# Performance work log

Measured on AMD Instinct MI355X. Metric: run time of the kernel, lower is better.

The kernel has to match this reference:

```python
import jax, jax.numpy as jnp
import numpy as np

N = 100000      # kg_E, number of entities
D = 256         # rel_dim
E = 1600000     # total COO edges (all batches concatenated)


def setup_inputs() -> dict:
    key = jax.random.key(0)
    ks = jax.random.split(key, 8)
    right_embed = jax.random.normal(ks[0], (N, D), dtype=jnp.float32)
    W1 = jax.random.normal(ks[1], (D, D), dtype=jnp.float32) * 0.02
    Wr = jax.random.normal(ks[2], (D, D), dtype=jnp.float32) * 0.02
    br = jax.random.normal(ks[3], (D,), dtype=jnp.float32) * 0.02
    edge_vals = jax.random.uniform(ks[4], (E,), dtype=jnp.float32)  # 1/(deg+1) weights
    edge_rows = jnp.sort(jax.random.randint(ks[5], (E,), 0, N))
    edge_cols = jax.random.randint(ks[6], (E,), 0, N)
    perm = jax.random.randint(ks[7], (N,), 0, N)  # ent_newid_tensor
    return {"right_embed": right_embed, "W1": W1, "Wr": Wr, "br": br,
            "edge_vals": edge_vals, "edge_rows": edge_rows,
            "edge_cols": edge_cols, "perm": perm}


def reference(right_embed, W1, Wr, br, edge_vals, edge_rows, edge_cols, perm):
    # add_diag_layer: dense transform then normalized-adjacency SpMM + ReLU
    h = right_embed @ W1                                   # [N, D]
    msg = edge_vals[:, None] * h[edge_cols]                # [E, D] gather
    agg = jax.ops.segment_sum(msg, edge_rows, num_segments=N)  # scatter-add
    gcn_e_1 = jax.nn.relu(agg)                             # [N, D]
    # highway gate blend with permuted input embeddings
    left = right_embed[perm]                               # [N, D]
    gate = jax.nn.sigmoid(left @ Wr + br)                  # [N, D]
    return gate * gcn_e_1 + (1.0 - gate) * left
```

## Files before the change

### kernel.cpp

```cpp
#include <hip/hip_runtime.h>
#include <hip/hip_bf16.h>
#include <math.h>

#define D 256

typedef short s16x8 __attribute__((ext_vector_type(8)));
typedef float f32x4 __attribute__((ext_vector_type(4)));

__device__ __forceinline__ unsigned short f2bf(float f) {
    unsigned int u = __builtin_bit_cast(unsigned int, f);
    unsigned int r = (u + 0x7fffu + ((u >> 16) & 1u)) >> 16;
    return (unsigned short)r;
}
__device__ __forceinline__ float bf2f(unsigned short s) {
    unsigned int u = ((unsigned int)s) << 16;
    return __builtin_bit_cast(float, u);
}

__global__ void swizzle_w(const float* __restrict__ W1, const float* __restrict__ Wr,
                          unsigned short* __restrict__ W1sw, unsigned short* __restrict__ Wrsw) {
    int idx = blockIdx.x * blockDim.x + threadIdx.x;
    int m = idx >> 16;
    int t = idx & 65535;
    const float* src = m ? Wr : W1;
    unsigned short* dst = m ? Wrsw : W1sw;
    int j = t & 7, lane = (t >> 3) & 63, nt = (t >> 9) & 15, kt = t >> 13;
    int k = kt * 32 + (lane >> 4) * 8 + j;
    int n = nt * 16 + (lane & 15);
    dst[t] = f2bf(src[k * D + n]);
}

__global__ void build_row_ptr(const int* __restrict__ rows, int* __restrict__ rp, int N, int E) {
    int r = blockIdx.x * blockDim.x + threadIdx.x;
    if (r > N) return;
    int lo = 0, hi = E;
    while (lo < hi) {
        int mid = (lo + hi) >> 1;
        if (rows[mid] < r) lo = mid + 1; else hi = mid;
    }
    rp[r] = lo;
}


__device__ __forceinline__ void stage_a_frag(const float* __restrict__ Xrow, int k0,
                                             unsigned short* __restrict__ lA, int fgi) {
    float4 f0 = *(const float4*)(Xrow + k0);
    float4 f1 = *(const float4*)(Xrow + k0 + 4);
    s16x8 sf;
    sf[0] = (short)f2bf(f0.x); sf[1] = (short)f2bf(f0.y);
    sf[2] = (short)f2bf(f0.z); sf[3] = (short)f2bf(f0.w);
    sf[4] = (short)f2bf(f1.x); sf[5] = (short)f2bf(f1.y);
    sf[6] = (short)f2bf(f1.z); sf[7] = (short)f2bf(f1.w);
    *(s16x8*)(lA + (size_t)fgi * 8) = sf;
}

__global__ __launch_bounds__(512) void gemm1_b(const float* __restrict__ X,
                                               const unsigned short* __restrict__ Wsw,
                                               unsigned short* __restrict__ h,
                                               int N, int numTiles) {
    __shared__ unsigned short lA[2 * 8 * 64 * 8];
    int t = threadIdx.x;
    int lane = t & 63;
    int wave = t >> 6;
    int quad = lane >> 4;

    s16x8 bfr[2][8];
#pragma unroll
    for (int ntl = 0; ntl < 2; ntl++) {
        int nt = wave * 2 + ntl;
#pragma unroll
        for (int kt = 0; kt < 8; kt++)
            bfr[ntl][kt] = *(const s16x8*)(Wsw + ((size_t)((kt * 16 + nt) * 64 + lane)) * 8);
    }

    for (int tile = blockIdx.x; tile < numTiles; tile += gridDim.x) {
#pragma unroll
        for (int q = 0; q < 2; q++) {
            int fgi = q * 512 + t;
            int mt = fgi >> 9, kt = (fgi >> 6) & 7, ll = fgi & 63;
            int rl = ll & 15, qd = ll >> 4;
            int grow = tile * 32 + mt * 16 + rl;
            if (grow >= N) grow = N - 1;
            stage_a_frag(X + (size_t)grow * D, kt * 32 + qd * 8, lA, fgi);
        }
        __syncthreads();

        f32x4 acc[2][2];
#pragma unroll
        for (int mt = 0; mt < 2; mt++)
#pragma unroll
            for (int ntl = 0; ntl < 2; ntl++) acc[mt][ntl] = (f32x4){0.f, 0.f, 0.f, 0.f};

#pragma unroll
        for (int mt = 0; mt < 2; mt++)
#pragma unroll
            for (int kt = 0; kt < 8; kt++) {
                s16x8 a = *(const s16x8*)(lA + (size_t)(((mt * 8 + kt) * 64 + lane)) * 8);
                acc[mt][0] = __builtin_amdgcn_mfma_f32_16x16x32_bf16(a, bfr[0][kt], acc[mt][0], 0, 0, 0);
                acc[mt][1] = __builtin_amdgcn_mfma_f32_16x16x32_bf16(a, bfr[1][kt], acc[mt][1], 0, 0, 0);
            }

#pragma unroll
        for (int mt = 0; mt < 2; mt++)
#pragma unroll
            for (int ntl = 0; ntl < 2; ntl++) {
                int col = (wave * 2 + ntl) * 16 + (lane & 15);
#pragma unroll
                for (int r = 0; r < 4; r++) {
                    int grow = tile * 32 + mt * 16 + quad * 4 + r;
                    if (grow < N) h[(size_t)grow * D + col] = f2bf(acc[mt][ntl][r]);
                }
            }
        __syncthreads();
    }
}

__global__ __launch_bounds__(512) void gemm2_b(const float* __restrict__ X,
                                               const int* __restrict__ perm,
                                               const unsigned short* __restrict__ Wsw,
                                               const float* __restrict__ br,
                                               const unsigned short* __restrict__ agg,
                                               float* __restrict__ out,
                                               int N, int numTiles) {
    __shared__ unsigned short lA[2 * 8 * 64 * 8];
    int t = threadIdx.x;
    int lane = t & 63;
    int wave = t >> 6;
    int quad = lane >> 4;

    s16x8 bfr[2][8];
#pragma unroll
    for (int ntl = 0; ntl < 2; ntl++) {
        int nt = wave * 2 + ntl;
#pragma unroll
        for (int kt = 0; kt < 8; kt++)
            bfr[ntl][kt] = *(const s16x8*)(Wsw + ((size_t)((kt * 16 + nt) * 64 + lane)) * 8);
    }

    for (int tile = blockIdx.x; tile < numTiles; tile += gridDim.x) {
#pragma unroll
        for (int q = 0; q < 2; q++) {
            int fgi = q * 512 + t;
            int mt = fgi >> 9, kt = (fgi >> 6) & 7, ll = fgi & 63;
            int rl = ll & 15, qd = ll >> 4;
            int grow = tile * 32 + mt * 16 + rl;
            if (grow >= N) grow = N - 1;
            int pr = perm[grow];
            stage_a_frag(X + (size_t)pr * D, kt * 32 + qd * 8, lA, fgi);
        }
        __syncthreads();

        f32x4 acc[2][2];
#pragma unroll
        for (int mt = 0; mt < 2; mt++)
#pragma unroll
            for (int ntl = 0; ntl < 2; ntl++) acc[mt][ntl] = (f32x4){0.f, 0.f, 0.f, 0.f};

#pragma unroll
        for (int mt = 0; mt < 2; mt++)
#pragma unroll
            for (int kt = 0; kt < 8; kt++) {
                s16x8 a = *(const s16x8*)(lA + (size_t)(((mt * 8 + kt) * 64 + lane)) * 8);
                acc[mt][0] = __builtin_amdgcn_mfma_f32_16x16x32_bf16(a, bfr[0][kt], acc[mt][0], 0, 0, 0);
                acc[mt][1] = __builtin_amdgcn_mfma_f32_16x16x32_bf16(a, bfr[1][kt], acc[mt][1], 0, 0, 0);
            }

#pragma unroll
        for (int mt = 0; mt < 2; mt++) {
#pragma unroll
            for (int ntl = 0; ntl < 2; ntl++) {
                int col = (wave * 2 + ntl) * 16 + (lane & 15);
                float b = br[col];
                int kt2 = col >> 5, qd2 = (col >> 3) & 3, j2 = col & 7;
#pragma unroll
                for (int r = 0; r < 4; r++) {
                    int rt = mt * 16 + quad * 4 + r;
                    int grow = tile * 32 + rt;
                    if (grow < N) {
                        float pre = acc[mt][ntl][r] + b;
                        float gate = 1.f / (1.f + __expf(-pre));
                        float gcn = bf2f(agg[(size_t)grow * D + col]);
                        float left = bf2f(lA[(size_t)(((mt * 8 + kt2) * 64 + qd2 * 16 + (rt & 15))) * 8 + j2]);
                        out[(size_t)grow * D + col] = gate * gcn + (1.f - gate) * left;
                    }
                }
            }
        }
        __syncthreads();
    }
}

__device__ __forceinline__ void acc4(float4& a, uint2 u, float v) {
    float x0 = __builtin_bit_cast(float, u.x << 16);
    float x1 = __builtin_bit_cast(float, u.x & 0xffff0000u);
    float x2 = __builtin_bit_cast(float, u.y << 16);
    float x3 = __builtin_bit_cast(float, u.y & 0xffff0000u);
    a.x += v * x0; a.y += v * x1; a.z += v * x2; a.w += v * x3;
}

__global__ __launch_bounds__(256) void scatter2(const uint2* __restrict__ hp,
                                                const int* __restrict__ rp,
                                                const int* __restrict__ cols,
                                                const float* __restrict__ vals,
                                                uint2* __restrict__ aggp,
                                                int N, int E) {
    int lane = threadIdx.x & 63;
    int wave = threadIdx.x >> 6;
    int row = blockIdx.x * 4 + wave;
    if (row >= N) return;
    int start = rp[row], end = rp[row + 1];

    float4 a = {0.f, 0.f, 0.f, 0.f};
    for (int base = start; base < end; base += 64) {
        int ii = base + lane;
        int iic = ii < E ? ii : E - 1;
        int cl = cols[iic];
        int vbits = __builtin_bit_cast(int, vals[iic]);
        int n = end - base; if (n > 64) n = 64;
        int i = 0;
        for (; i + 8 <= n; i += 8) {
            uint2 u[8]; float vv[8];
#pragma unroll
            for (int k = 0; k < 8; k++) {
                int c = __builtin_amdgcn_readlane(cl, i + k);
                vv[k] = __builtin_bit_cast(float, __builtin_amdgcn_readlane(vbits, i + k));
                u[k] = hp[(size_t)c * 64 + lane];
            }
#pragma unroll
            for (int k = 0; k < 8; k++) acc4(a, u[k], vv[k]);
        }
        for (; i < n; i++) {
            int c = __builtin_amdgcn_readlane(cl, i);
            float v = __builtin_bit_cast(float, __builtin_amdgcn_readlane(vbits, i));
            uint2 u = hp[(size_t)c * 64 + lane];
            acc4(a, u, v);
        }
    }
    a.x = fmaxf(a.x, 0.f); a.y = fmaxf(a.y, 0.f);
    a.z = fmaxf(a.z, 0.f); a.w = fmaxf(a.w, 0.f);
    uint2 o;
    o.x = (unsigned int)f2bf(a.x) | ((unsigned int)f2bf(a.y) << 16);
    o.y = (unsigned int)f2bf(a.z) | ((unsigned int)f2bf(a.w) << 16);
    aggp[(size_t)row * 64 + lane] = o;
}

extern "C" void kernel_launch(void* const* d_in, const int* in_sizes, int n_in,
                              void* d_out, int out_size, void* d_ws, size_t ws_size,
                              hipStream_t stream) {
    const float* right = (const float*)d_in[0];
    const float* W1    = (const float*)d_in[1];
    const float* Wr    = (const float*)d_in[2];
    const float* br    = (const float*)d_in[3];
    const float* evals = (const float*)d_in[4];
    const int*   erows = (const int*)d_in[5];
    const int*   ecols = (const int*)d_in[6];
    const int*   perm  = (const int*)d_in[7];
    int N = in_sizes[7];
    int E = in_sizes[4];
    float* out = (float*)d_out;

    char* ws = (char*)d_ws;
    unsigned short* W1sw = (unsigned short*)ws;
    unsigned short* Wrsw = W1sw + D * D;
    int* rp = (int*)(ws + (size_t)2 * D * D * 2);
    size_t off = (size_t)2 * D * D * 2 + 4 * (size_t)(N + 1);
    off = (off + 255) & ~(size_t)255;
    unsigned short* h = (unsigned short*)(ws + off);
    unsigned short* agg = h + (size_t)N * D;

    int numTiles = (N + 31) / 32;

    swizzle_w<<<512, 256, 0, stream>>>(W1, Wr, W1sw, Wrsw);
    build_row_ptr<<<(N + 256) / 256, 256, 0, stream>>>(erows, rp, N, E);
    gemm1_b<<<numTiles, 512, 0, stream>>>(right, W1sw, h, N, numTiles);
    scatter2<<<(N + 3) / 4, 256, 0, stream>>>((const uint2*)h, rp, ecols, evals,
                                              (uint2*)agg, N, E);
    gemm2_b<<<numTiles, 512, 0, stream>>>(right, perm, Wrsw, br, agg, out, N, numTiles);
}
```

Before: 417.1 us.

## Store h and agg in column-group-major layout and scatter per column group

The intermediate h and agg buffers change from row-major to 16 column groups of 16 bf16 values each, stored group-major. The SpMM kernel is split so each block handles one column group, with eight edges per wave processed in parallel and combined by a shuffle reduction. Block IDs are interleaved so groups map to different XCDs, keeping each group's 3.2 MB slice of h in L2. Each gather now moves 32 bytes per edge instead of 512, at the cost of reading the edge arrays 16 times and extra shuffle work. The GEMM grids are also capped at 768 persistent blocks.

Result: slower. 633.5 us (+51.9%).

```diff
diff --git a/kernel.cpp b/kernel.cpp
--- a/kernel.cpp
+++ b/kernel.cpp
@@ -104,11 +104,13 @@
         for (int mt = 0; mt < 2; mt++)
 #pragma unroll
             for (int ntl = 0; ntl < 2; ntl++) {
-                int col = (wave * 2 + ntl) * 16 + (lane & 15);
+                int g = wave * 2 + ntl;
+                int c = lane & 15;
 #pragma unroll
                 for (int r = 0; r < 4; r++) {
                     int grow = tile * 32 + mt * 16 + quad * 4 + r;
-                    if (grow < N) h[(size_t)grow * D + col] = f2bf(acc[mt][ntl][r]);
+                    if (grow < N)
+                        h[(size_t)g * N * 16 + (size_t)grow * 16 + c] = f2bf(acc[mt][ntl][r]);
                 }
             }
         __syncthreads();
@@ -169,7 +171,9 @@
         for (int mt = 0; mt < 2; mt++) {
 #pragma unroll
             for (int ntl = 0; ntl < 2; ntl++) {
-                int col = (wave * 2 + ntl) * 16 + (lane & 15);
+                int g = wave * 2 + ntl;
+                int cc = lane & 15;
+                int col = g * 16 + cc;
                 float b = br[col];
                 int kt2 = col >> 5, qd2 = (col >> 3) & 3, j2 = col & 7;
 #pragma unroll
@@ -179,7 +183,7 @@
                     if (grow < N) {
                         float pre = acc[mt][ntl][r] + b;
                         float gate = 1.f / (1.f + __expf(-pre));
-                        float gcn = bf2f(agg[(size_t)grow * D + col]);
+                        float gcn = bf2f(agg[(size_t)g * N * 16 + (size_t)grow * 16 + cc]);
                         float left = bf2f(lA[(size_t)(((mt * 8 + kt2) * 64 + qd2 * 16 + (rt & 15))) * 8 + j2]);
                         out[(size_t)grow * D + col] = gate * gcn + (1.f - gate) * left;
                     }
@@ -190,58 +194,55 @@
     }
 }
 
-__device__ __forceinline__ void acc4(float4& a, uint2 u, float v) {
-    float x0 = __builtin_bit_cast(float, u.x << 16);
-    float x1 = __builtin_bit_cast(float, u.x & 0xffff0000u);
-    float x2 = __builtin_bit_cast(float, u.y << 16);
-    float x3 = __builtin_bit_cast(float, u.y & 0xffff0000u);
-    a.x += v * x0; a.y += v * x1; a.z += v * x2; a.w += v * x3;
-}
-
-__global__ __launch_bounds__(256) void scatter2(const uint2* __restrict__ hp,
+__global__ __launch_bounds__(256) void scatter3(const unsigned int* __restrict__ hg,
                                                 const int* __restrict__ rp,
                                                 const int* __restrict__ cols,
                                                 const float* __restrict__ vals,
-                                                uint2* __restrict__ aggp,
-                                                int N, int E) {
+                                                unsigned int* __restrict__ aggg,
+                                                int N, int E, int BPG) {
+    int bid = blockIdx.x;
+    int x = bid & 7;
+    int j = bid >> 3;
+    int hi = (j >= BPG) ? 1 : 0;
+    int g = 2 * x + hi;
+    int bg = j - hi * BPG;
+    int wave = threadIdx.x >> 6;
     int lane = threadIdx.x & 63;
-    int wave = threadIdx.x >> 6;
-    int row = blockIdx.x * 4 + wave;
-    if (row >= N) return;
-    int start = rp[row], end = rp[row + 1];
-
-    float4 a = {0.f, 0.f, 0.f, 0.f};
-    for (int base = start; base < end; base += 64) {
-        int ii = base + lane;
-        int iic = ii < E ? ii : E - 1;
-        int cl = cols[iic];
-        int vbits = __builtin_bit_cast(int, vals[iic]);
-        int n = end - base; if (n > 64) n = 64;
-        int i = 0;
-        for (; i + 8 <= n; i += 8) {
-            uint2 u[8]; float vv[8];
-#pragma unroll
-            for (int k = 0; k < 8; k++) {
-                int c = __builtin_amdgcn_readlane(cl, i + k);
-                vv[k] = __builtin_bit_cast(float, __builtin_amdgcn_readlane(vbits, i + k));
-                u[k] = hp[(size_t)c * 64 + lane];
-            }
-#pragma unroll
-            for (int k = 0; k < 8; k++) acc4(a, u[k], vv[k]);
-        }
-        for (; i < n; i++) {
-            int c = __builtin_amdgcn_readlane(cl, i);
-            float v = __builtin_bit_cast(float, __builtin_amdgcn_readlane(vbits, i));
-            uint2 u = hp[(size_t)c * 64 + lane];
-            acc4(a, u, v);
-        }
-    }
-    a.x = fmaxf(a.x, 0.f); a.y = fmaxf(a.y, 0.f);
-    a.z = fmaxf(a.z, 0.f); a.w = fmaxf(a.w, 0.f);
-    uint2 o;
-    o.x = (unsigned int)f2bf(a.x) | ((unsigned int)f2bf(a.y) << 16);
-    o.y = (unsigned int)f2bf(a.z) | ((unsigned int)f2bf(a.w) << 16);
-    aggp[(size_t)row * 64 + lane] = o;
+    int s = lane >> 3;
+    int ci = lane & 7;
+    const unsigned int* hbase = hg + (size_t)g * N * 8;
+    unsigned int* abase = aggg + (size_t)g * N * 8;
+    int stride = BPG * 4;
+    for (int row = bg * 4 + wave; row < N; row += stride) {
+        int start = rp[row], end = rp[row + 1];
+        float a0 = 0.f, a1 = 0.f;
+        for (int base = start; base < end; base += 64) {
+            int ii = base + lane;
+            int iic = ii < E ? ii : E - 1;
+            int cl = cols[iic];
+            int vb = __builtin_bit_cast(int, vals[iic]);
+            int n = end - base; if (n > 64) n = 64;
+            for (int i = 0; i < n; i += 8) {
+                int idx = (i + s) << 2;
+                int c = __builtin_amdgcn_ds_bpermute(idx, cl);
+                int vvb = __builtin_amdgcn_ds_bpermute(idx, vb);
+                float v = (i + s) < n ? __builtin_bit_cast(float, vvb) : 0.f;
+                unsigned int u = hbase[(size_t)c * 8 + ci];
+                float x0 = __builtin_bit_cast(float, u << 16);
+                float x1 = __builtin_bit_cast(float, u & 0xffff0000u);
+                a0 += v * x0;
+                a1 += v * x1;
+            }
+        }
+        a0 += __shfl_xor(a0, 8, 64);  a1 += __shfl_xor(a1, 8, 64);
+        a0 += __shfl_xor(a0, 16, 64); a1 += __shfl_xor(a1, 16, 64);
+        a0 += __shfl_xor(a0, 32, 64); a1 += __shfl_xor(a1, 32, 64);
+        if (s == 0) {
+            a0 = fmaxf(a0, 0.f); a1 = fmaxf(a1, 0.f);
+            unsigned int o = (unsigned int)f2bf(a0) | ((unsigned int)f2bf(a1) << 16);
+            abase[(size_t)row * 8 + ci] = o;
+        }
+    }
 }
 
 extern "C" void kernel_launch(void* const* d_in, const int* in_sizes, int n_in,
@@ -269,11 +270,13 @@
     unsigned short* agg = h + (size_t)N * D;
 
     int numTiles = (N + 31) / 32;
+    int gemmGrid = numTiles < 768 ? numTiles : 768;
+    int BPG = 1024;
 
     swizzle_w<<<512, 256, 0, stream>>>(W1, Wr, W1sw, Wrsw);
     build_row_ptr<<<(N + 256) / 256, 256, 0, stream>>>(erows, rp, N, E);
-    gemm1_b<<<numTiles, 512, 0, stream>>>(right, W1sw, h, N, numTiles);
-    scatter2<<<(N + 3) / 4, 256, 0, stream>>>((const uint2*)h, rp, ecols, evals,
-                                              (uint2*)agg, N, E);
-    gemm2_b<<<numTiles, 512, 0, stream>>>(right, perm, Wrsw, br, agg, out, N, numTiles);
-}
+    gemm1_b<<<gemmGrid, 512, 0, stream>>>(right, W1sw, h, N, numTiles);
+    scatter3<<<16 * BPG, 256, 0, stream>>>((const unsigned int*)h, rp, ecols, evals,
+                                           (unsigned int*)agg, N, E, BPG);
+    gemm2_b<<<gemmGrid, 512, 0, stream>>>(right, perm, Wrsw, br, agg, out, N, numTiles);
+}
```

## Pre-pack bf16 A tiles and double-buffer them into LDS with async loads

Applied to the files above, without the earlier changes.

Adds a pack_x kernel that converts the fp32 input rows (gathered through perm for the gate GEMM) into bf16 MFMA-fragment-ordered tiles in workspace. Both GEMMs become persistent kernels with a grid capped at 512 that stream these packed tiles into double-buffered LDS using global_load_lds, so the next tile's load overlaps the current tile's MFMAs. The goal is to hide load latency and drop per-tile conversion and perm indexing from the GEMM loops. In exchange it adds two extra kernels and an extra write and read of a bf16 copy of the input, with workspace buffers aliased to hold it.

New measurement: 413.9 us. No clear change (-0.8%).

```diff
diff --git a/kernel.cpp b/kernel.cpp
--- a/kernel.cpp
+++ b/kernel.cpp
@@ -15,6 +15,12 @@
 __device__ __forceinline__ float bf2f(unsigned short s) {
     unsigned int u = ((unsigned int)s) << 16;
     return __builtin_bit_cast(float, u);
+}
+
+__device__ __forceinline__ void gl_lds16(const unsigned short* g, unsigned short* l) {
+    __builtin_amdgcn_global_load_lds(
+        (const __attribute__((address_space(1))) unsigned int*)g,
+        (__attribute__((address_space(3))) unsigned int*)l, 16, 0, 0);
 }
 
 __global__ void swizzle_w(const float* __restrict__ W1, const float* __restrict__ Wr,
@@ -41,9 +47,8 @@
     rp[r] = lo;
 }
 
-
 __device__ __forceinline__ void stage_a_frag(const float* __restrict__ Xrow, int k0,
-                                             unsigned short* __restrict__ lA, int fgi) {
+                                             unsigned short* __restrict__ dst, int fgi) {
     float4 f0 = *(const float4*)(Xrow + k0);
     float4 f1 = *(const float4*)(Xrow + k0 + 4);
     s16x8 sf;
@@ -51,18 +56,35 @@
     sf[2] = (short)f2bf(f0.z); sf[3] = (short)f2bf(f0.w);
     sf[4] = (short)f2bf(f1.x); sf[5] = (short)f2bf(f1.y);
     sf[6] = (short)f2bf(f1.z); sf[7] = (short)f2bf(f1.w);
-    *(s16x8*)(lA + (size_t)fgi * 8) = sf;
-}
-
-__global__ __launch_bounds__(512) void gemm1_b(const float* __restrict__ X,
+    *(s16x8*)(dst + (size_t)fgi * 8) = sf;
+}
+
+__global__ __launch_bounds__(256) void pack_x(const float* __restrict__ X,
+                                              const int* __restrict__ perm,
+                                              unsigned short* __restrict__ Xp,
+                                              int N, int numTiles) {
+    int idx = blockIdx.x * 256 + threadIdx.x;
+    int total = numTiles << 10;
+    if (idx >= total) return;
+    int fgi = idx & 1023, tile = idx >> 10;
+    int mt = fgi >> 9, kt = (fgi >> 6) & 7, ll = fgi & 63;
+    int rl = ll & 15, qd = ll >> 4;
+    int grow = tile * 32 + mt * 16 + rl;
+    if (grow >= N) grow = N - 1;
+    int row = perm ? perm[grow] : grow;
+    stage_a_frag(X + (size_t)row * D, kt * 32 + qd * 8, Xp, idx);
+}
+
+__global__ __launch_bounds__(512) void gemm1_p(const unsigned short* __restrict__ Xp,
                                                const unsigned short* __restrict__ Wsw,
                                                unsigned short* __restrict__ h,
                                                int N, int numTiles) {
-    __shared__ unsigned short lA[2 * 8 * 64 * 8];
+    __shared__ __attribute__((aligned(16))) unsigned short lA[2][8192];
     int t = threadIdx.x;
     int lane = t & 63;
     int wave = t >> 6;
     int quad = lane >> 4;
+    if ((int)blockIdx.x >= numTiles) return;
 
     s16x8 bfr[2][8];
 #pragma unroll
@@ -73,17 +95,26 @@
             bfr[ntl][kt] = *(const s16x8*)(Wsw + ((size_t)((kt * 16 + nt) * 64 + lane)) * 8);
     }
 
-    for (int tile = blockIdx.x; tile < numTiles; tile += gridDim.x) {
-#pragma unroll
-        for (int q = 0; q < 2; q++) {
-            int fgi = q * 512 + t;
-            int mt = fgi >> 9, kt = (fgi >> 6) & 7, ll = fgi & 63;
-            int rl = ll & 15, qd = ll >> 4;
-            int grow = tile * 32 + mt * 16 + rl;
-            if (grow >= N) grow = N - 1;
-            stage_a_frag(X + (size_t)grow * D, kt * 32 + qd * 8, lA, fgi);
-        }
-        __syncthreads();
+    int stride = gridDim.x;
+    int ti = blockIdx.x;
+    {
+        const unsigned short* src = Xp + (size_t)ti * 8192;
+        gl_lds16(src + wave * 512 + lane * 8, &lA[0][wave * 512]);
+        gl_lds16(src + (wave + 8) * 512 + lane * 8, &lA[0][(wave + 8) * 512]);
+    }
+    int cur = 0;
+    for (; ti < numTiles; ti += stride) {
+        int nxt = ti + stride;
+        if (nxt < numTiles) {
+            const unsigned short* src = Xp + (size_t)nxt * 8192;
+            gl_lds16(src + wave * 512 + lane * 8, &lA[cur ^ 1][wave * 512]);
+            gl_lds16(src + (wave + 8) * 512 + lane * 8, &lA[cur ^ 1][(wave + 8) * 512]);
+            asm volatile("s_waitcnt vmcnt(2)" ::: "memory");
+        } else {
+            asm volatile("s_waitcnt vmcnt(0)" ::: "memory");
+        }
+        __builtin_amdgcn_s_barrier();
+        __builtin_amdgcn_sched_barrier(0);
 
         f32x4 acc[2][2];
 #pragma unroll
@@ -95,7 +126,7 @@
         for (int mt = 0; mt < 2; mt++)
 #pragma unroll
             for (int kt = 0; kt < 8; kt++) {
-                s16x8 a = *(const s16x8*)(lA + (size_t)(((mt * 8 + kt) * 64 + lane)) * 8);
+                s16x8 a = *(const s16x8*)(&lA[cur][(size_t)(((mt * 8 + kt) * 64 + lane)) * 8]);
                 acc[mt][0] = __builtin_amdgcn_mfma_f32_16x16x32_bf16(a, bfr[0][kt], acc[mt][0], 0, 0, 0);
                 acc[mt][1] = __builtin_amdgcn_mfma_f32_16x16x32_bf16(a, bfr[1][kt], acc[mt][1], 0, 0, 0);
             }
@@ -107,26 +138,27 @@
                 int col = (wave * 2 + ntl) * 16 + (lane & 15);
 #pragma unroll
                 for (int r = 0; r < 4; r++) {
-                    int grow = tile * 32 + mt * 16 + quad * 4 + r;
+                    int grow = ti * 32 + mt * 16 + quad * 4 + r;
                     if (grow < N) h[(size_t)grow * D + col] = f2bf(acc[mt][ntl][r]);
                 }
             }
-        __syncthreads();
-    }
-}
-
-__global__ __launch_bounds__(512) void gemm2_b(const float* __restrict__ X,
-                                               const int* __restrict__ perm,
+        __builtin_amdgcn_s_barrier();
+        cur ^= 1;
+    }
+}
+
+__global__ __launch_bounds__(512) void gemm2_p(const unsigned short* __restrict__ Xp,
                                                const unsigned short* __restrict__ Wsw,
                                                const float* __restrict__ br,
                                                const unsigned short* __restrict__ agg,
                                                float* __restrict__ out,
                                                int N, int numTiles) {
-    __shared__ unsigned short lA[2 * 8 * 64 * 8];
+    __shared__ __attribute__((aligned(16))) unsigned short lA[2][8192];
     int t = threadIdx.x;
     int lane = t & 63;
     int wave = t >> 6;
     int quad = lane >> 4;
+    if ((int)blockIdx.x >= numTiles) return;
 
     s16x8 bfr[2][8];
 #pragma unroll
@@ -137,18 +169,26 @@
             bfr[ntl][kt] = *(const s16x8*)(Wsw + ((size_t)((kt * 16 + nt) * 64 + lane)) * 8);
     }
 
-    for (int tile = blockIdx.x; tile < numTiles; tile += gridDim.x) {
-#pragma unroll
-        for (int q = 0; q < 2; q++) {
-            int fgi = q * 512 + t;
-            int mt = fgi >> 9, kt = (fgi >> 6) & 7, ll = fgi & 63;
-            int rl = ll & 15, qd = ll >> 4;
-            int grow = tile * 32 + mt * 16 + rl;
-            if (grow >= N) grow = N - 1;
-            int pr = perm[grow];
-            stage_a_frag(X + (size_t)pr * D, kt * 32 + qd * 8, lA, fgi);
-        }
-        __syncthreads();
+    int stride = gridDim.x;
+    int ti = blockIdx.x;
+    {
+        const unsigned short* src = Xp + (size_t)ti * 8192;
+        gl_lds16(src + wave * 512 + lane * 8, &lA[0][wave * 512]);
+        gl_lds16(src + (wave + 8) * 512 + lane * 8, &lA[0][(wave + 8) * 512]);
+    }
+    int cur = 0;
+    for (; ti < numTiles; ti += stride) {
+        int nxt = ti + stride;
+        if (nxt < numTiles) {
+            const unsigned short* src = Xp + (size_t)nxt * 8192;
+            gl_lds16(src + wave * 512 + lane * 8, &lA[cur ^ 1][wave * 512]);
+            gl_lds16(src + (wave + 8) * 512 + lane * 8, &lA[cur ^ 1][(wave + 8) * 512]);
+            asm volatile("s_waitcnt vmcnt(2)" ::: "memory");
+        } else {
+            asm volatile("s_waitcnt vmcnt(0)" ::: "memory");
+        }
+        __builtin_amdgcn_s_barrier();
+        __builtin_amdgcn_sched_barrier(0);
 
         f32x4 acc[2][2];
 #pragma unroll
@@ -160,7 +200,7 @@
         for (int mt = 0; mt < 2; mt++)
 #pragma unroll
             for (int kt = 0; kt < 8; kt++) {
-                s16x8 a = *(const s16x8*)(lA + (size_t)(((mt * 8 + kt) * 64 + lane)) * 8);
+                s16x8 a = *(const s16x8*)(&lA[cur][(size_t)(((mt * 8 + kt) * 64 + lane)) * 8]);
                 acc[mt][0] = __builtin_amdgcn_mfma_f32_16x16x32_bf16(a, bfr[0][kt], acc[mt][0], 0, 0, 0);
                 acc[mt][1] = __builtin_amdgcn_mfma_f32_16x16x32_bf16(a, bfr[1][kt], acc[mt][1], 0, 0, 0);
             }
@@ -175,18 +215,19 @@
 #pragma unroll
                 for (int r = 0; r < 4; r++) {
                     int rt = mt * 16 + quad * 4 + r;
-                    int grow = tile * 32 + rt;
+                    int grow = ti * 32 + rt;
                     if (grow < N) {
                         float pre = acc[mt][ntl][r] + b;
                         float gate = 1.f / (1.f + __expf(-pre));
                         float gcn = bf2f(agg[(size_t)grow * D + col]);
-                        float left = bf2f(lA[(size_t)(((mt * 8 + kt2) * 64 + qd2 * 16 + (rt & 15))) * 8 + j2]);
+                        float left = bf2f(lA[cur][(size_t)(((mt * 8 + kt2) * 64 + qd2 * 16 + (rt & 15))) * 8 + j2]);
                         out[(size_t)grow * D + col] = gate * gcn + (1.f - gate) * left;
                     }
                 }
             }
         }
-        __syncthreads();
+        __builtin_amdgcn_s_barrier();
+        cur ^= 1;
     }
 }
 
@@ -259,6 +300,9 @@
     int E = in_sizes[4];
     float* out = (float*)d_out;
 
+    int numTiles = (N + 31) / 32;
+    size_t tileBytes = (size_t)numTiles * 16384;
+
     char* ws = (char*)d_ws;
     unsigned short* W1sw = (unsigned short*)ws;
     unsigned short* Wrsw = W1sw + D * D;
@@ -266,14 +310,19 @@
     size_t off = (size_t)2 * D * D * 2 + 4 * (size_t)(N + 1);
     off = (off + 255) & ~(size_t)255;
     unsigned short* h = (unsigned short*)(ws + off);
-    unsigned short* agg = h + (size_t)N * D;
-
-    int numTiles = (N + 31) / 32;
+    unsigned short* Xp2 = h;
+    unsigned short* Xp1 = (unsigned short*)(ws + off + tileBytes);
+    unsigned short* agg = Xp1;
+
+    int packBlocks = (numTiles * 1024 + 255) / 256;
+    int gemmGrid = numTiles < 512 ? numTiles : 512;
 
     swizzle_w<<<512, 256, 0, stream>>>(W1, Wr, W1sw, Wrsw);
     build_row_ptr<<<(N + 256) / 256, 256, 0, stream>>>(erows, rp, N, E);
-    gemm1_b<<<numTiles, 512, 0, stream>>>(right, W1sw, h, N, numTiles);
+    pack_x<<<packBlocks, 256, 0, stream>>>(right, (const int*)nullptr, Xp1, N, numTiles);
+    gemm1_p<<<gemmGrid, 512, 0, stream>>>(Xp1, W1sw, h, N, numTiles);
     scatter2<<<(N + 3) / 4, 256, 0, stream>>>((const uint2*)h, rp, ecols, evals,
                                               (uint2*)agg, N, E);
-    gemm2_b<<<numTiles, 512, 0, stream>>>(right, perm, Wrsw, br, agg, out, N, numTiles);
-}
+    pack_x<<<packBlocks, 256, 0, stream>>>(right, perm, Xp2, N, numTiles);
+    gemm2_p<<<gemmGrid, 512, 0, stream>>>(Xp2, W1sw == nullptr ? nullptr : Wrsw, br, agg, out, N, numTiles);
+}
```

## Fuse SpMM aggregation into gate GEMM kernel and merge preprocessing kernels

Applied to the files above, without the earlier changes.

The CSR gather/scatter aggregation moves into the gate GEMM kernel. Each 512-thread block computes its 32 output rows' aggregation into shared memory (fp32) and then blends them with the gate without writing or rereading a bf16 agg buffer. The weight swizzle and row-pointer build are merged into one launch to cut launch overhead. In exchange, each block has more shared memory and serial per-wave work (4 rows per wave, processed one after another), which may lower occupancy and latency hiding for the gather.

Result: faster. 403.2 us (-3.3%).

```diff
diff --git a/kernel.cpp b/kernel.cpp
--- a/kernel.cpp
+++ b/kernel.cpp
@@ -17,30 +17,31 @@
     return __builtin_bit_cast(float, u);
 }
 
-__global__ void swizzle_w(const float* __restrict__ W1, const float* __restrict__ Wr,
-                          unsigned short* __restrict__ W1sw, unsigned short* __restrict__ Wrsw) {
-    int idx = blockIdx.x * blockDim.x + threadIdx.x;
-    int m = idx >> 16;
-    int t = idx & 65535;
-    const float* src = m ? Wr : W1;
-    unsigned short* dst = m ? Wrsw : W1sw;
-    int j = t & 7, lane = (t >> 3) & 63, nt = (t >> 9) & 15, kt = t >> 13;
-    int k = kt * 32 + (lane >> 4) * 8 + j;
-    int n = nt * 16 + (lane & 15);
-    dst[t] = f2bf(src[k * D + n]);
-}
-
-__global__ void build_row_ptr(const int* __restrict__ rows, int* __restrict__ rp, int N, int E) {
-    int r = blockIdx.x * blockDim.x + threadIdx.x;
-    if (r > N) return;
-    int lo = 0, hi = E;
-    while (lo < hi) {
-        int mid = (lo + hi) >> 1;
-        if (rows[mid] < r) lo = mid + 1; else hi = mid;
-    }
-    rp[r] = lo;
-}
-
+__global__ void pre_k(const float* __restrict__ W1, const float* __restrict__ Wr,
+                      unsigned short* __restrict__ W1sw, unsigned short* __restrict__ Wrsw,
+                      const int* __restrict__ rows, int* __restrict__ rp, int N, int E) {
+    int bid = blockIdx.x;
+    if (bid < 512) {
+        int idx = bid * 256 + threadIdx.x;
+        int m = idx >> 16;
+        int t = idx & 65535;
+        const float* src = m ? Wr : W1;
+        unsigned short* dst = m ? Wrsw : W1sw;
+        int j = t & 7, lane = (t >> 3) & 63, nt = (t >> 9) & 15, kt = t >> 13;
+        int k = kt * 32 + (lane >> 4) * 8 + j;
+        int n = nt * 16 + (lane & 15);
+        dst[t] = f2bf(src[k * D + n]);
+    } else {
+        int r = (bid - 512) * 256 + threadIdx.x;
+        if (r > N) return;
+        int lo = 0, hi = E;
+        while (lo < hi) {
+            int mid = (lo + hi) >> 1;
+            if (rows[mid] < r) lo = mid + 1; else hi = mid;
+        }
+        rp[r] = lo;
+    }
+}
 
 __device__ __forceinline__ void stage_a_frag(const float* __restrict__ Xrow, int k0,
                                              unsigned short* __restrict__ lA, int fgi) {
@@ -115,81 +116,6 @@
     }
 }
 
-__global__ __launch_bounds__(512) void gemm2_b(const float* __restrict__ X,
-                                               const int* __restrict__ perm,
-                                               const unsigned short* __restrict__ Wsw,
-                                               const float* __restrict__ br,
-                                               const unsigned short* __restrict__ agg,
-                                               float* __restrict__ out,
-                                               int N, int numTiles) {
-    __shared__ unsigned short lA[2 * 8 * 64 * 8];
-    int t = threadIdx.x;
-    int lane = t & 63;
-    int wave = t >> 6;
-    int quad = lane >> 4;
-
-    s16x8 bfr[2][8];
-#pragma unroll
-    for (int ntl = 0; ntl < 2; ntl++) {
-        int nt = wave * 2 + ntl;
-#pragma unroll
-        for (int kt = 0; kt < 8; kt++)
-            bfr[ntl][kt] = *(const s16x8*)(Wsw + ((size_t)((kt * 16 + nt) * 64 + lane)) * 8);
-    }
-
-    for (int tile = blockIdx.x; tile < numTiles; tile += gridDim.x) {
-#pragma unroll
-        for (int q = 0; q < 2; q++) {
-            int fgi = q * 512 + t;
-            int mt = fgi >> 9, kt = (fgi >> 6) & 7, ll = fgi & 63;
-            int rl = ll & 15, qd = ll >> 4;
-            int grow = tile * 32 + mt * 16 + rl;
-            if (grow >= N) grow = N - 1;
-            int pr = perm[grow];
-            stage_a_frag(X + (size_t)pr * D, kt * 32 + qd * 8, lA, fgi);
-        }
-        __syncthreads();
-
-        f32x4 acc[2][2];
-#pragma unroll
-        for (int mt = 0; mt < 2; mt++)
-#pragma unroll
-            for (int ntl = 0; ntl < 2; ntl++) acc[mt][ntl] = (f32x4){0.f, 0.f, 0.f, 0.f};
-
-#pragma unroll
-        for (int mt = 0; mt < 2; mt++)
-#pragma unroll
-            for (int kt = 0; kt < 8; kt++) {
-                s16x8 a = *(const s16x8*)(lA + (size_t)(((mt * 8 + kt) * 64 + lane)) * 8);
-                acc[mt][0] = __builtin_amdgcn_mfma_f32_16x16x32_bf16(a, bfr[0][kt], acc[mt][0], 0, 0, 0);
-                acc[mt][1] = __builtin_amdgcn_mfma_f32_16x16x32_bf16(a, bfr[1][kt], acc[mt][1], 0, 0, 0);
-            }
-
-#pragma unroll
-        for (int mt = 0; mt < 2; mt++) {
-#pragma unroll
-            for (int ntl = 0; ntl < 2; ntl++) {
-                int col = (wave * 2 + ntl) * 16 + (lane & 15);
-                float b = br[col];
-                int kt2 = col >> 5, qd2 = (col >> 3) & 3, j2 = col & 7;
-#pragma unroll
-                for (int r = 0; r < 4; r++) {
-                    int rt = mt * 16 + quad * 4 + r;
-                    int grow = tile * 32 + rt;
-                    if (grow < N) {
-                        float pre = acc[mt][ntl][r] + b;
-                        float gate = 1.f / (1.f + __expf(-pre));
-                        float gcn = bf2f(agg[(size_t)grow * D + col]);
-                        float left = bf2f(lA[(size_t)(((mt * 8 + kt2) * 64 + qd2 * 16 + (rt & 15))) * 8 + j2]);
-                        out[(size_t)grow * D + col] = gate * gcn + (1.f - gate) * left;
-                    }
-                }
-            }
-        }
-        __syncthreads();
-    }
-}
-
 __device__ __forceinline__ void acc4(float4& a, uint2 u, float v) {
     float x0 = __builtin_bit_cast(float, u.x << 16);
     float x1 = __builtin_bit_cast(float, u.x & 0xffff0000u);
@@ -198,50 +124,119 @@
     a.x += v * x0; a.y += v * x1; a.z += v * x2; a.w += v * x3;
 }
 
-__global__ __launch_bounds__(256) void scatter2(const uint2* __restrict__ hp,
-                                                const int* __restrict__ rp,
-                                                const int* __restrict__ cols,
-                                                const float* __restrict__ vals,
-                                                uint2* __restrict__ aggp,
-                                                int N, int E) {
-    int lane = threadIdx.x & 63;
-    int wave = threadIdx.x >> 6;
-    int row = blockIdx.x * 4 + wave;
-    if (row >= N) return;
-    int start = rp[row], end = rp[row + 1];
-
-    float4 a = {0.f, 0.f, 0.f, 0.f};
-    for (int base = start; base < end; base += 64) {
-        int ii = base + lane;
-        int iic = ii < E ? ii : E - 1;
-        int cl = cols[iic];
-        int vbits = __builtin_bit_cast(int, vals[iic]);
-        int n = end - base; if (n > 64) n = 64;
-        int i = 0;
-        for (; i + 8 <= n; i += 8) {
-            uint2 u[8]; float vv[8];
-#pragma unroll
-            for (int k = 0; k < 8; k++) {
-                int c = __builtin_amdgcn_readlane(cl, i + k);
-                vv[k] = __builtin_bit_cast(float, __builtin_amdgcn_readlane(vbits, i + k));
-                u[k] = hp[(size_t)c * 64 + lane];
-            }
-#pragma unroll
-            for (int k = 0; k < 8; k++) acc4(a, u[k], vv[k]);
-        }
-        for (; i < n; i++) {
-            int c = __builtin_amdgcn_readlane(cl, i);
-            float v = __builtin_bit_cast(float, __builtin_amdgcn_readlane(vbits, i));
-            uint2 u = hp[(size_t)c * 64 + lane];
-            acc4(a, u, v);
-        }
-    }
-    a.x = fmaxf(a.x, 0.f); a.y = fmaxf(a.y, 0.f);
-    a.z = fmaxf(a.z, 0.f); a.w = fmaxf(a.w, 0.f);
-    uint2 o;
-    o.x = (unsigned int)f2bf(a.x) | ((unsigned int)f2bf(a.y) << 16);
-    o.y = (unsigned int)f2bf(a.z) | ((unsigned int)f2bf(a.w) << 16);
-    aggp[(size_t)row * 64 + lane] = o;
+__global__ __launch_bounds__(512, 4) void gemm2_f(const float* __restrict__ X,
+                                                  const int* __restrict__ perm,
+                                                  const unsigned short* __restrict__ Wsw,
+                                                  const float* __restrict__ br,
+                                                  const uint2* __restrict__ hp,
+                                                  const int* __restrict__ rp,
+                                                  const int* __restrict__ cols,
+                                                  const float* __restrict__ vals,
+                                                  float* __restrict__ out,
+                                                  int N, int E, int numTiles) {
+    __shared__ unsigned short lA[2 * 8 * 64 * 8];
+    __shared__ __attribute__((aligned(16))) float lAgg[32][260];
+    int t = threadIdx.x;
+    int lane = t & 63;
+    int wave = t >> 6;
+    int quad = lane >> 4;
+    int tile = blockIdx.x;
+    if (tile >= numTiles) return;
+
+#pragma unroll
+    for (int q = 0; q < 2; q++) {
+        int fgi = q * 512 + t;
+        int mt = fgi >> 9, kt = (fgi >> 6) & 7, ll = fgi & 63;
+        int rl = ll & 15, qd = ll >> 4;
+        int grow = tile * 32 + mt * 16 + rl;
+        if (grow >= N) grow = N - 1;
+        int pr = perm[grow];
+        stage_a_frag(X + (size_t)pr * D, kt * 32 + qd * 8, lA, fgi);
+    }
+
+    s16x8 bfr[2][8];
+#pragma unroll
+    for (int ntl = 0; ntl < 2; ntl++) {
+        int nt = wave * 2 + ntl;
+#pragma unroll
+        for (int kt = 0; kt < 8; kt++)
+            bfr[ntl][kt] = *(const s16x8*)(Wsw + ((size_t)((kt * 16 + nt) * 64 + lane)) * 8);
+    }
+    __syncthreads();
+
+    f32x4 acc[2][2];
+#pragma unroll
+    for (int mt = 0; mt < 2; mt++)
+#pragma unroll
+        for (int ntl = 0; ntl < 2; ntl++) acc[mt][ntl] = (f32x4){0.f, 0.f, 0.f, 0.f};
+
+#pragma unroll
+    for (int mt = 0; mt < 2; mt++)
+#pragma unroll
+        for (int kt = 0; kt < 8; kt++) {
+            s16x8 a = *(const s16x8*)(lA + (size_t)(((mt * 8 + kt) * 64 + lane)) * 8);
+            acc[mt][0] = __builtin_amdgcn_mfma_f32_16x16x32_bf16(a, bfr[0][kt], acc[mt][0], 0, 0, 0);
+            acc[mt][1] = __builtin_amdgcn_mfma_f32_16x16x32_bf16(a, bfr[1][kt], acc[mt][1], 0, 0, 0);
+        }
+
+#pragma unroll 1
+    for (int rr = 0; rr < 4; rr++) {
+        int row = tile * 32 + wave * 4 + rr;
+        if (row >= N) break;
+        int start = rp[row], end = rp[row + 1];
+        float4 a = {0.f, 0.f, 0.f, 0.f};
+        for (int base = start; base < end; base += 64) {
+            int ii = base + lane;
+            int iic = ii < E ? ii : E - 1;
+            int cl = cols[iic];
+            int vbits = __builtin_bit_cast(int, vals[iic]);
+            int n = end - base; if (n > 64) n = 64;
+            int i = 0;
+            for (; i + 8 <= n; i += 8) {
+                uint2 u[8]; float vv[8];
+#pragma unroll
+                for (int k = 0; k < 8; k++) {
+                    int c = __builtin_amdgcn_readlane(cl, i + k);
+                    vv[k] = __builtin_bit_cast(float, __builtin_amdgcn_readlane(vbits, i + k));
+                    u[k] = hp[(size_t)c * 64 + lane];
+                }
+#pragma unroll
+                for (int k = 0; k < 8; k++) acc4(a, u[k], vv[k]);
+            }
+            for (; i < n; i++) {
+                int c = __builtin_amdgcn_readlane(cl, i);
+                float v = __builtin_bit_cast(float, __builtin_amdgcn_readlane(vbits, i));
+                uint2 u = hp[(size_t)c * 64 + lane];
+                acc4(a, u, v);
+            }
+        }
+        a.x = fmaxf(a.x, 0.f); a.y = fmaxf(a.y, 0.f);
+        a.z = fmaxf(a.z, 0.f); a.w = fmaxf(a.w, 0.f);
+        *(float4*)(&lAgg[wave * 4 + rr][lane * 4]) = a;
+    }
+    __syncthreads();
+
+#pragma unroll
+    for (int mt = 0; mt < 2; mt++) {
+#pragma unroll
+        for (int ntl = 0; ntl < 2; ntl++) {
+            int col = (wave * 2 + ntl) * 16 + (lane & 15);
+            float b = br[col];
+            int kt2 = col >> 5, qd2 = (col >> 3) & 3, j2 = col & 7;
+#pragma unroll
+            for (int r = 0; r < 4; r++) {
+                int rt = mt * 16 + quad * 4 + r;
+                int grow = tile * 32 + rt;
+                if (grow < N) {
+                    float pre = acc[mt][ntl][r] + b;
+                    float gate = 1.f / (1.f + __expf(-pre));
+                    float gcn = lAgg[rt][col];
+                    float left = bf2f(lA[(size_t)(((mt * 8 + kt2) * 64 + qd2 * 16 + (rt & 15))) * 8 + j2]);
+                    out[(size_t)grow * D + col] = gate * gcn + (1.f - gate) * left;
+                }
+            }
+        }
+    }
 }
 
 extern "C" void kernel_launch(void* const* d_in, const int* in_sizes, int n_in,
@@ -266,14 +261,12 @@
     size_t off = (size_t)2 * D * D * 2 + 4 * (size_t)(N + 1);
     off = (off + 255) & ~(size_t)255;
     unsigned short* h = (unsigned short*)(ws + off);
-    unsigned short* agg = h + (size_t)N * D;
 
     int numTiles = (N + 31) / 32;
-
-    swizzle_w<<<512, 256, 0, stream>>>(W1, Wr, W1sw, Wrsw);
-    build_row_ptr<<<(N + 256) / 256, 256, 0, stream>>>(erows, rp, N, E);
+    int rpBlocks = (N + 256) / 256;
+
+    pre_k<<<512 + rpBlocks, 256, 0, stream>>>(W1, Wr, W1sw, Wrsw, erows, rp, N, E);
     gemm1_b<<<numTiles, 512, 0, stream>>>(right, W1sw, h, N, numTiles);
-    scatter2<<<(N + 3) / 4, 256, 0, stream>>>((const uint2*)h, rp, ecols, evals,
-                                              (uint2*)agg, N, E);
-    gemm2_b<<<numTiles, 512, 0, stream>>>(right, perm, Wrsw, br, agg, out, N, numTiles);
-}
+    gemm2_f<<<numTiles, 512, 0, stream>>>(right, perm, Wrsw, br, (const uint2*)h,
+                                          rp, ecols, evals, out, N, E, numTiles);
+}
```
